# Kernel tuning notes

Measured on AMD Instinct MI355X. Metric: run time of the kernel, lower is better.

Reference implementation:

```python
import jax, jax.numpy as jnp
import numpy as np
import math

B, S, H, NH = 2, 2048, 1024, 16
DK = H // NH
EPS = 1e-5

def setup_inputs() -> dict:
    key = jax.random.key(0)
    ks = jax.random.split(key, 8)
    sd = 0.02
    return {
        "x": jax.random.normal(ks[0], (B, S, H), dtype=jnp.float32),
        "ln1_w": jnp.ones((H,), jnp.float32),
        "ln1_b": jnp.zeros((H,), jnp.float32),
        "W_qkv": jax.random.normal(ks[1], (H, 3 * H), jnp.float32) * sd,
        "b_qkv": jnp.zeros((3 * H,), jnp.float32),
        "W_o": jax.random.normal(ks[2], (H, H), jnp.float32) * sd,
        "b_o": jnp.zeros((H,), jnp.float32),
        "ln2_w": jnp.ones((H,), jnp.float32),
        "ln2_b": jnp.zeros((H,), jnp.float32),
        "W_fc": jax.random.normal(ks[3], (H, 4 * H), jnp.float32) * sd,
        "b_fc": jnp.zeros((4 * H,), jnp.float32),
        "W_proj": jax.random.normal(ks[4], (4 * H, H), jnp.float32) * sd,
        "b_proj": jnp.zeros((H,), jnp.float32),
    }

def _layernorm(x, w, b):
    mu = jnp.mean(x, axis=-1, keepdims=True)
    var = jnp.mean(jnp.square(x - mu), axis=-1, keepdims=True)
    return (x - mu) * jax.lax.rsqrt(var + EPS) * w + b

def _attn(x, W_qkv, b_qkv, W_o, b_o):
    bs, seq, _ = x.shape
    qkv = x @ W_qkv + b_qkv                      # [b,s,3H]
    q, k, v = jnp.split(qkv, 3, axis=-1)
    q = q.reshape(bs, seq, NH, DK).transpose(0, 2, 1, 3)  # [b,h,s,d]
    k = k.reshape(bs, seq, NH, DK).transpose(0, 2, 1, 3)
    v = v.reshape(bs, seq, NH, DK).transpose(0, 2, 1, 3)
    scores = jnp.einsum("bhqd,bhkd->bhqk", q, k) / math.sqrt(DK)
    causal = jnp.tril(jnp.ones((seq, seq), bool))
    scores = jnp.where(causal, scores, -jnp.inf)
    attn = jax.nn.softmax(scores, axis=-1)
    out = jnp.einsum("bhqk,bhkd->bhqd", attn, v)
    out = out.transpose(0, 2, 1, 3).reshape(bs, seq, H)
    return out @ W_o + b_o

def reference(x, ln1_w, ln1_b, W_qkv, b_qkv, W_o, b_o, ln2_w, ln2_b, W_fc, b_fc, W_proj, b_proj):
    x = x + _attn(_layernorm(x, ln1_w, ln1_b), W_qkv, b_qkv, W_o, b_o)
    h = _layernorm(x, ln2_w, ln2_b)
    h = jax.nn.gelu(h @ W_fc + b_fc, approximate=False) @ W_proj + b_proj
    return x + h
```

## Files before the change

### kernel.cpp

```cpp
#include <hip/hip_runtime.h>
#include <hip/hip_bf16.h>
#include <math.h>

#define H_DIM 1024
#define SEQ   2048
#define BATCH 2
#define NHEAD 16
#define DKV   64
#define ROWS  (BATCH*SEQ)
#define QSCALE 0.18033688f

typedef __attribute__((ext_vector_type(8))) short short8;
typedef __attribute__((ext_vector_type(4))) float f32x4;

static __device__ __forceinline__ unsigned short f32_bf16(float f) {
    unsigned int u = __builtin_bit_cast(unsigned int, f);
    u += 0x7FFF + ((u >> 16) & 1);
    return (unsigned short)(u >> 16);
}

static __device__ __forceinline__ float fast_erf(float x) {
    float ax = fabsf(x);
    float t = 1.0f / fmaf(0.3275911f, ax, 1.0f);
    float p = t * fmaf(t, fmaf(t, fmaf(t, fmaf(t, 1.061405429f, -1.453152027f),
                                       1.421413741f), -0.284496736f), 0.254829592f);
    float y = fmaf(-p, __expf(-ax * ax), 1.0f);
    return copysignf(y, x);
}

static __device__ __forceinline__ void gload16(const unsigned short* g, unsigned short* l) {
    __builtin_amdgcn_global_load_lds(
        (const __attribute__((address_space(1))) void*)g,
        (__attribute__((address_space(3))) void*)l,
        16, 0, 0);
}

__global__ __launch_bounds__(256) void transpose_bf16(const float* __restrict__ in,
                                                      unsigned short* __restrict__ out,
                                                      int K, int N) {
    __shared__ float tile[32][33];
    int n0 = blockIdx.x * 32, k0 = blockIdx.y * 32;
    int tx = threadIdx.x & 31, ty = threadIdx.x >> 5;
    #pragma unroll
    for (int i = 0; i < 4; ++i)
        tile[ty + i * 8][tx] = in[(size_t)(k0 + ty + i * 8) * N + n0 + tx];
    __syncthreads();
    #pragma unroll
    for (int i = 0; i < 4; ++i)
        out[(size_t)(n0 + ty + i * 8) * K + k0 + tx] = f32_bf16(tile[tx][ty + i * 8]);
}

__global__ __launch_bounds__(256) void ln_bf16(const float* __restrict__ x,
                                               const float* __restrict__ w,
                                               const float* __restrict__ bb,
                                               unsigned short* __restrict__ out) {
    int row = blockIdx.x;
    int tid = threadIdx.x;
    float4 v = ((const float4*)(x + (size_t)row * H_DIM))[tid];
    float s  = v.x + v.y + v.z + v.w;
    float s2 = v.x*v.x + v.y*v.y + v.z*v.z + v.w*v.w;
    #pragma unroll
    for (int off = 1; off < 64; off <<= 1) {
        s  += __shfl_xor(s,  off, 64);
        s2 += __shfl_xor(s2, off, 64);
    }
    __shared__ float red[8];
    int wv = tid >> 6;
    if ((tid & 63) == 0) { red[wv] = s; red[4 + wv] = s2; }
    __syncthreads();
    s  = red[0] + red[1] + red[2] + red[3];
    s2 = red[4] + red[5] + red[6] + red[7];
    float mu = s * (1.0f / H_DIM);
    float rs = rsqrtf(s2 * (1.0f / H_DIM) - mu * mu + 1e-5f);
    float4 wv4 = ((const float4*)w)[tid];
    float4 bv4 = ((const float4*)bb)[tid];
    ushort4 o;
    o.x = f32_bf16((v.x - mu) * rs * wv4.x + bv4.x);
    o.y = f32_bf16((v.y - mu) * rs * wv4.y + bv4.y);
    o.z = f32_bf16((v.z - mu) * rs * wv4.z + bv4.z);
    o.w = f32_bf16((v.w - mu) * rs * wv4.w + bv4.w);
    ((ushort4*)(out + (size_t)row * H_DIM))[tid] = o;
}

template<int EPI>
static __device__ __forceinline__ void epi_store(f32x4 a, int row0, int col, int N,
                                                 const float* __restrict__ bias,
                                                 const float* __restrict__ resid,
                                                 float* __restrict__ outF,
                                                 unsigned short* __restrict__ outH,
                                                 unsigned short* __restrict__ outH2) {
    float bv = bias[col];
    if (EPI == 4 && col >= 2048) {
        int bb = row0 >> 11, ss = row0 & 2047;
        int hd = col - 2048;
        ushort4 u;
        u.x = f32_bf16(a[0] + bv);
        u.y = f32_bf16(a[1] + bv);
        u.z = f32_bf16(a[2] + bv);
        u.w = f32_bf16(a[3] + bv);
        *(ushort4*)&outH2[((size_t)bb * 1024 + hd) * SEQ + ss] = u;
    } else {
        #pragma unroll
        for (int j = 0; j < 4; ++j) {
            int row = row0 + j;
            size_t idx = (size_t)row * N + col;
            float c = a[j] + bv;
            if (EPI == 0) {
                outF[idx] = c;
            } else if (EPI == 1) {
                outF[idx] = resid[idx] + c;
            } else if (EPI == 2) {
                float g = 0.5f * c * (1.0f + fast_erf(c * 0.70710678118f));
                outH[idx] = f32_bf16(g);
            } else if (EPI == 3) {
                outH[idx] = f32_bf16(c);
            } else {
                float c2 = (col < 1024) ? c * QSCALE : c;
                outH[(size_t)row * 2048 + col] = f32_bf16(c2);
            }
        }
    }
}

template<int EPI, int NI>
__global__ __launch_bounds__(256) void gemmT(const unsigned short* __restrict__ A,
                                             const unsigned short* __restrict__ Bt,
                                             const float* __restrict__ bias,
                                             const float* __restrict__ resid,
                                             float* __restrict__ outF,
                                             unsigned short* __restrict__ outH,
                                             unsigned short* __restrict__ outH2,
                                             int gx, int N, int K) {
    constexpr int BN = NI * 32;
    __shared__ __attribute__((aligned(16))) unsigned short As[128][64];
    __shared__ __attribute__((aligned(16))) unsigned short Bs[BN][64];
    int tid = threadIdx.x;
    int w = tid >> 6, l = tid & 63;
    int l15 = l & 15, lg = l >> 4;
    int wm = w & 1, wn = w >> 1;

    int qq = gridDim.x >> 3;
    int wg = (blockIdx.x & 7) * qq + (blockIdx.x >> 3);
    int bm = wg / gx, bn = wg - bm * gx;
    int m0 = bm * 128, n0 = bn * BN;

    f32x4 acc[4][NI] = {};

    const unsigned short* aptr[4];
    unsigned short* lA[4];
    #pragma unroll
    for (int j = 0; j < 4; ++j) {
        int slot = (w * 4 + j) * 64 + l;
        int row = slot >> 3;
        int lchunk = (slot & 7) ^ (row & 7);
        aptr[j] = A + (size_t)(m0 + row) * K + lchunk * 8;
        lA[j] = &As[0][0] + (w * 4 + j) * 512;
    }
    const unsigned short* bptr[NI];
    unsigned short* lB[NI];
    #pragma unroll
    for (int j = 0; j < NI; ++j) {
        int slot = (w * NI + j) * 64 + l;
        int row = slot >> 3;
        int lchunk = (slot & 7) ^ (row & 7);
        bptr[j] = Bt + (size_t)(n0 + row) * K + lchunk * 8;
        lB[j] = &Bs[0][0] + (w * NI + j) * 512;
    }
    int swz[2];
    swz[0] = ((0 + lg) ^ (l15 & 7)) * 8;
    swz[1] = ((4 + lg) ^ (l15 & 7)) * 8;
    const unsigned short* pA = &As[wm * 64 + l15][0];
    const unsigned short* pB = &Bs[wn * (NI * 16) + l15][0];

    for (int k0 = 0; k0 < K; k0 += 64) {
        __syncthreads();
        #pragma unroll
        for (int j = 0; j < 4; ++j) gload16(aptr[j] + k0, lA[j]);
        #pragma unroll
        for (int j = 0; j < NI; ++j) gload16(bptr[j] + k0, lB[j]);
        __syncthreads();

        #pragma unroll
        for (int ks = 0; ks < 2; ++ks) {
            short8 af[4], bf[NI];
            #pragma unroll
            for (int mi = 0; mi < 4; ++mi)
                af[mi] = *(const short8*)(pA + mi * 16 * 64 + swz[ks]);
            #pragma unroll
            for (int ni = 0; ni < NI; ++ni)
                bf[ni] = *(const short8*)(pB + ni * 16 * 64 + swz[ks]);
            #pragma unroll
            for (int mi = 0; mi < 4; ++mi)
                #pragma unroll
                for (int ni = 0; ni < NI; ++ni)
                    acc[mi][ni] = __builtin_amdgcn_mfma_f32_16x16x32_bf16(af[mi], bf[ni], acc[mi][ni], 0, 0, 0);
        }
    }

    #pragma unroll
    for (int mi = 0; mi < 4; ++mi)
        #pragma unroll
        for (int ni = 0; ni < NI; ++ni)
            epi_store<EPI>(acc[mi][ni], m0 + wm * 64 + mi * 16 + lg * 4,
                           n0 + wn * (NI * 16) + ni * 16 + l15, N, bias, resid, outF, outH, outH2);
}

__global__ __launch_bounds__(512) void attn_mfma(const unsigned short* __restrict__ qk,
                                                 const unsigned short* __restrict__ vT,
                                                 unsigned short* __restrict__ out) {
    int bid = blockIdx.x;
    int swz = (bid & 7) * 64 + (bid >> 3);
    int b  = swz >> 8;
    int h  = (swz >> 4) & 15;
    int qt = 15 - (swz & 15);
    int tid = threadIdx.x;
    int w = tid >> 6, l = tid & 63;
    int l15 = l & 15, lg = l >> 4;

    __shared__ __attribute__((aligned(16))) unsigned short Ks[64][72];
    __shared__ __attribute__((aligned(16))) unsigned short Vt[64][72];
    __shared__ __attribute__((aligned(16))) unsigned short Ps[8][16][72];

    int qrow = qt * 128 + w * 16 + l15;
    short8 qf[2];
    {
        const unsigned short* qp = qk + (size_t)(b * SEQ + qrow) * 2048 + h * DKV + lg * 8;
        qf[0] = *(const short8*)qp;
        qf[1] = *(const short8*)(qp + 32);
    }
    short8 vf5;
    #pragma unroll
    for (int i = 0; i < 8; ++i) vf5[i] = (l15 == 0) ? (short)0x3F80 : (short)0;

    int srow = tid >> 3;
    int scol = (tid & 7) * 8;
    const unsigned short* kbase = qk + (size_t)(b * SEQ + srow) * 2048 + 1024 + h * DKV + scol;
    const unsigned short* vbase = vT + ((size_t)(b * NHEAD + h) * DKV + srow) * SEQ + scol;

    short8 kr = *(const short8*)kbase;
    short8 vr = *(const short8*)vbase;

    float m = -1e30f;
    f32x4 oacc[4] = {};
    f32x4 oext = {};

    int nt = 2 * qt + 2;
    for (int kt = 0; kt < nt; ++kt) {
        __syncthreads();
        *(short8*)&Ks[srow][scol] = kr;
        *(short8*)&Vt[srow][scol] = vr;
        __syncthreads();
        if (kt + 1 < nt) {
            kr = *(const short8*)(kbase + (size_t)(kt + 1) * 64 * 2048);
            vr = *(const short8*)(vbase + (kt + 1) * 64);
        }

        f32x4 sc[4] = {};
        __builtin_amdgcn_s_setprio(1);
        #pragma unroll
        for (int dstep = 0; dstep < 2; ++dstep) {
            #pragma unroll
            for (int st = 0; st < 4; ++st) {
                short8 kf = *(const short8*)&Ks[st * 16 + l15][dstep * 32 + lg * 8];
                sc[st] = __builtin_amdgcn_mfma_f32_16x16x32_bf16(kf, qf[dstep], sc[st], 0, 0, 0);
            }
        }
        __builtin_amdgcn_s_setprio(0);

        int klim = qrow - kt * 64;
        float pv[4][4];
        float pmax = -1e30f;
        #pragma unroll
        for (int st = 0; st < 4; ++st) {
            #pragma unroll
            for (int j = 0; j < 4; ++j) {
                float s = sc[st][j];
                if (st * 16 + lg * 4 + j > klim) s = -1e30f;
                pv[st][j] = s;
                pmax = fmaxf(pmax, s);
            }
        }

        if (!__all(pmax - m <= 8.0f)) {
            float pr = fmaxf(pmax, __shfl_xor(pmax, 16, 64));
            pr = fmaxf(pr, __shfl_xor(pr, 32, 64));
            float mn = fmaxf(m, pr);
            float scl = exp2f(m - mn);
            #pragma unroll
            for (int d = 0; d < 4; ++d)
                #pragma unroll
                for (int j = 0; j < 4; ++j)
                    oacc[d][j] *= scl;
            #pragma unroll
            for (int j = 0; j < 4; ++j) oext[j] *= scl;
            m = mn;
        }

        #pragma unroll
        for (int st = 0; st < 4; ++st) {
            float p0 = exp2f(pv[st][0] - m);
            float p1 = exp2f(pv[st][1] - m);
            float p2 = exp2f(pv[st][2] - m);
            float p3 = exp2f(pv[st][3] - m);
            unsigned int ua, ub;
            asm("v_cvt_pk_bf16_f32 %0, %1, %2" : "=v"(ua) : "v"(p0), "v"(p1));
            asm("v_cvt_pk_bf16_f32 %0, %1, %2" : "=v"(ub) : "v"(p2), "v"(p3));
            uint2 u = make_uint2(ua, ub);
            *(uint2*)&Ps[w][l15][st * 16 + lg * 4] = u;
        }

        __builtin_amdgcn_s_setprio(1);
        #pragma unroll
        for (int ks = 0; ks < 2; ++ks) {
            short8 pf = *(const short8*)&Ps[w][l15][ks * 32 + lg * 8];
            #pragma unroll
            for (int d = 0; d < 4; ++d) {
                short8 vf = *(const short8*)&Vt[d * 16 + l15][ks * 32 + lg * 8];
                oacc[d] = __builtin_amdgcn_mfma_f32_16x16x32_bf16(vf, pf, oacc[d], 0, 0, 0);
            }
            oext = __builtin_amdgcn_mfma_f32_16x16x32_bf16(vf5, pf, oext, 0, 0, 0);
        }
        __builtin_amdgcn_s_setprio(0);
    }

    float lsum = __shfl(oext[0], l15, 64);
    float inv = 1.0f / lsum;
    size_t ob = (size_t)(b * SEQ + qrow) * H_DIM + h * DKV;
    #pragma unroll
    for (int d = 0; d < 4; ++d) {
        ushort4 u;
        #pragma unroll
        for (int j = 0; j < 4; ++j)
            ((unsigned short*)&u)[j] = f32_bf16(oacc[d][j] * inv);
        *(ushort4*)&out[ob + d * 16 + lg * 4] = u;
    }
}

extern "C" void kernel_launch(void* const* d_in, const int* in_sizes, int n_in,
                              void* d_out, int out_size, void* d_ws, size_t ws_size,
                              hipStream_t stream) {
    const float* x     = (const float*)d_in[0];
    const float* ln1w  = (const float*)d_in[1];
    const float* ln1b  = (const float*)d_in[2];
    const float* Wqkv  = (const float*)d_in[3];
    const float* bqkv  = (const float*)d_in[4];
    const float* Wo    = (const float*)d_in[5];
    const float* bo    = (const float*)d_in[6];
    const float* ln2w  = (const float*)d_in[7];
    const float* ln2b  = (const float*)d_in[8];
    const float* Wfc   = (const float*)d_in[9];
    const float* bfc   = (const float*)d_in[10];
    const float* Wproj = (const float*)d_in[11];
    const float* bproj = (const float*)d_in[12];
    float* out = (float*)d_out;

    char* ws = (char*)d_ws;
    size_t off = 0;
    auto take = [&](size_t bytes) {
        void* p = ws + off;
        off += (bytes + 255) & ~(size_t)255;
        return p;
    };

    unsigned short* WqT  = (unsigned short*)take((size_t)3072 * 1024 * 2);
    unsigned short* WoT  = (unsigned short*)take((size_t)1024 * 1024 * 2);
    unsigned short* WfcT = (unsigned short*)take((size_t)4096 * 1024 * 2);
    unsigned short* WpT  = (unsigned short*)take((size_t)1024 * 4096 * 2);
    unsigned short* xn1   = (unsigned short*)take((size_t)ROWS * 1024 * 2);
    unsigned short* qk_h  = (unsigned short*)take((size_t)ROWS * 2048 * 2);
    unsigned short* vT    = (unsigned short*)take((size_t)ROWS * 1024 * 2);
    unsigned short* attn  = (unsigned short*)take((size_t)ROWS * 1024 * 2);
    float*          x1    = (float*)take((size_t)ROWS * 1024 * 4);
    unsigned short* xn2   = (unsigned short*)take((size_t)ROWS * 1024 * 2);
    unsigned short* hbuf  = (unsigned short*)take((size_t)ROWS * 4096 * 2);

    transpose_bf16<<<dim3(3072 / 32, 1024 / 32), 256, 0, stream>>>(Wqkv,  WqT,  1024, 3072);
    transpose_bf16<<<dim3(1024 / 32, 1024 / 32), 256, 0, stream>>>(Wo,    WoT,  1024, 1024);
    transpose_bf16<<<dim3(4096 / 32, 1024 / 32), 256, 0, stream>>>(Wfc,   WfcT, 1024, 4096);
    transpose_bf16<<<dim3(1024 / 32, 4096 / 32), 256, 0, stream>>>(Wproj, WpT,  4096, 1024);

    ln_bf16<<<ROWS, 256, 0, stream>>>(x, ln1w, ln1b, xn1);

    gemmT<4, 4><<<768, 256, 0, stream>>>(xn1, WqT, bqkv, nullptr, nullptr, qk_h, vT, 24, 3072, 1024);

    attn_mfma<<<512, 512, 0, stream>>>(qk_h, vT, attn);

    gemmT<1, 2><<<512, 256, 0, stream>>>(attn, WoT, bo, x, x1, nullptr, nullptr, 16, 1024, 1024);

    ln_bf16<<<ROWS, 256, 0, stream>>>(x1, ln2w, ln2b, xn2);

    gemmT<2, 4><<<1024, 256, 0, stream>>>(xn2, WfcT, bfc, nullptr, nullptr, hbuf, nullptr, 32, 4096, 1024);

    gemmT<1, 2><<<512, 256, 0, stream>>>(hbuf, WpT, bproj, x1, out, nullptr, nullptr, 16, 1024, 4096);
}
```

Baseline: 258.7 us.

## Use 8 waves per GEMM block with a 2x4 warp grid

Doubles the GEMM block from 256 to 512 threads, so each of the 8 waves computes a 64 x BN/4 sub-tile instead of 64 x BN/2. Global-to-LDS loads are spread across all 512 threads with fewer loads each. Per-wave accumulators and MFMA work are halved, which lowers register pressure and adds more waves to hide latency. The cost is more LDS fragment reads per MFMA, because each wave reuses its A fragments across fewer columns, and heavier barrier synchronisation.

New measurement: 248.8 us. 1.04x faster.

```diff
diff --git a/kernel.cpp b/kernel.cpp
--- a/kernel.cpp
+++ b/kernel.cpp
@@ -123,7 +123,7 @@
 }
 
 template<int EPI, int NI>
-__global__ __launch_bounds__(256) void gemmT(const unsigned short* __restrict__ A,
+__global__ __launch_bounds__(512) void gemmT(const unsigned short* __restrict__ A,
                                              const unsigned short* __restrict__ Bt,
                                              const float* __restrict__ bias,
                                              const float* __restrict__ resid,
@@ -132,6 +132,8 @@
                                              unsigned short* __restrict__ outH2,
                                              int gx, int N, int K) {
     constexpr int BN = NI * 32;
+    constexpr int WN = BN / 4;
+    constexpr int NT = WN / 16;
     __shared__ __attribute__((aligned(16))) unsigned short As[128][64];
     __shared__ __attribute__((aligned(16))) unsigned short Bs[BN][64];
     int tid = threadIdx.x;
@@ -144,55 +146,55 @@
     int bm = wg / gx, bn = wg - bm * gx;
     int m0 = bm * 128, n0 = bn * BN;
 
-    f32x4 acc[4][NI] = {};
-
-    const unsigned short* aptr[4];
-    unsigned short* lA[4];
-    #pragma unroll
-    for (int j = 0; j < 4; ++j) {
-        int slot = (w * 4 + j) * 64 + l;
+    f32x4 acc[4][NT] = {};
+
+    const unsigned short* aptr[2];
+    unsigned short* lA[2];
+    #pragma unroll
+    for (int j = 0; j < 2; ++j) {
+        int slot = j * 512 + tid;
         int row = slot >> 3;
         int lchunk = (slot & 7) ^ (row & 7);
         aptr[j] = A + (size_t)(m0 + row) * K + lchunk * 8;
-        lA[j] = &As[0][0] + (w * 4 + j) * 512;
-    }
-    const unsigned short* bptr[NI];
-    unsigned short* lB[NI];
-    #pragma unroll
-    for (int j = 0; j < NI; ++j) {
-        int slot = (w * NI + j) * 64 + l;
+        lA[j] = &As[0][0] + (size_t)slot * 8 - l * 8;
+    }
+    const unsigned short* bptr[NI / 2];
+    unsigned short* lB[NI / 2];
+    #pragma unroll
+    for (int j = 0; j < NI / 2; ++j) {
+        int slot = j * 512 + tid;
         int row = slot >> 3;
         int lchunk = (slot & 7) ^ (row & 7);
         bptr[j] = Bt + (size_t)(n0 + row) * K + lchunk * 8;
-        lB[j] = &Bs[0][0] + (w * NI + j) * 512;
+        lB[j] = &Bs[0][0] + (size_t)slot * 8 - l * 8;
     }
     int swz[2];
     swz[0] = ((0 + lg) ^ (l15 & 7)) * 8;
     swz[1] = ((4 + lg) ^ (l15 & 7)) * 8;
     const unsigned short* pA = &As[wm * 64 + l15][0];
-    const unsigned short* pB = &Bs[wn * (NI * 16) + l15][0];
+    const unsigned short* pB = &Bs[wn * WN + l15][0];
 
     for (int k0 = 0; k0 < K; k0 += 64) {
         __syncthreads();
         #pragma unroll
-        for (int j = 0; j < 4; ++j) gload16(aptr[j] + k0, lA[j]);
-        #pragma unroll
-        for (int j = 0; j < NI; ++j) gload16(bptr[j] + k0, lB[j]);
+        for (int j = 0; j < 2; ++j) gload16(aptr[j] + k0, lA[j]);
+        #pragma unroll
+        for (int j = 0; j < NI / 2; ++j) gload16(bptr[j] + k0, lB[j]);
         __syncthreads();
 
         #pragma unroll
         for (int ks = 0; ks < 2; ++ks) {
-            short8 af[4], bf[NI];
+            short8 af[4], bf[NT];
             #pragma unroll
             for (int mi = 0; mi < 4; ++mi)
                 af[mi] = *(const short8*)(pA + mi * 16 * 64 + swz[ks]);
             #pragma unroll
-            for (int ni = 0; ni < NI; ++ni)
+            for (int ni = 0; ni < NT; ++ni)
                 bf[ni] = *(const short8*)(pB + ni * 16 * 64 + swz[ks]);
             #pragma unroll
             for (int mi = 0; mi < 4; ++mi)
                 #pragma unroll
-                for (int ni = 0; ni < NI; ++ni)
+                for (int ni = 0; ni < NT; ++ni)
                     acc[mi][ni] = __builtin_amdgcn_mfma_f32_16x16x32_bf16(af[mi], bf[ni], acc[mi][ni], 0, 0, 0);
         }
     }
@@ -200,9 +202,9 @@
     #pragma unroll
     for (int mi = 0; mi < 4; ++mi)
         #pragma unroll
-        for (int ni = 0; ni < NI; ++ni)
+        for (int ni = 0; ni < NT; ++ni)
             epi_store<EPI>(acc[mi][ni], m0 + wm * 64 + mi * 16 + lg * 4,
-                           n0 + wn * (NI * 16) + ni * 16 + l15, N, bias, resid, outF, outH, outH2);
+                           n0 + wn * WN + ni * 16 + l15, N, bias, resid, outF, outH, outH2);
 }
 
 __global__ __launch_bounds__(512) void attn_mfma(const unsigned short* __restrict__ qk,
@@ -381,15 +383,15 @@
 
     ln_bf16<<<ROWS, 256, 0, stream>>>(x, ln1w, ln1b, xn1);
 
-    gemmT<4, 4><<<768, 256, 0, stream>>>(xn1, WqT, bqkv, nullptr, nullptr, qk_h, vT, 24, 3072, 1024);
+    gemmT<4, 4><<<768, 512, 0, stream>>>(xn1, WqT, bqkv, nullptr, nullptr, qk_h, vT, 24, 3072, 1024);
 
     attn_mfma<<<512, 512, 0, stream>>>(qk_h, vT, attn);
 
-    gemmT<1, 2><<<512, 256, 0, stream>>>(attn, WoT, bo, x, x1, nullptr, nullptr, 16, 1024, 1024);
+    gemmT<1, 2><<<512, 512, 0, stream>>>(attn, WoT, bo, x, x1, nullptr, nullptr, 16, 1024, 1024);
 
     ln_bf16<<<ROWS, 256, 0, stream>>>(x1, ln2w, ln2b, xn2);
 
-    gemmT<2, 4><<<1024, 256, 0, stream>>>(xn2, WfcT, bfc, nullptr, nullptr, hbuf, nullptr, 32, 4096, 1024);
-
-    gemmT<1, 2><<<512, 256, 0, stream>>>(hbuf, WpT, bproj, x1, out, nullptr, nullptr, 16, 1024, 4096);
-}
+    gemmT<2, 4><<<1024, 512, 0, stream>>>(xn2, WfcT, bfc, nullptr, nullptr, hbuf, nullptr, 32, 4096, 1024);
+
+    gemmT<1, 2><<<512, 512, 0, stream>>>(hbuf, WpT, bproj, x1, out, nullptr, nullptr, 16, 1024, 4096);
+}
```
